# Kernel optimization log

Measured on AMD Instinct MI355X. Metric: run time of the kernel, lower is better.

The kernel has to match this reference:

```python
import jax, jax.numpy as jnp
import numpy as np

NH, NL, NPT = 8, 4, 4  # num_heads, num_levels, num_points


def _bilinear_sample(feat, grid):
    # feat: [N, C, H, W]; grid: [N, S, 2] normalized coords, align_corners=True, zeros padding
    N, C, H, W = feat.shape
    x = (grid[..., 0] + 1.0) * 0.5 * (W - 1)
    y = (grid[..., 1] + 1.0) * 0.5 * (H - 1)
    x0 = jnp.floor(x)
    y0 = jnp.floor(y)
    x1 = x0 + 1.0
    y1 = y0 + 1.0
    wx1 = x - x0
    wx0 = 1.0 - wx1
    wy1 = y - y0
    wy0 = 1.0 - wy1
    flat = feat.reshape(N, C, H * W)

    def corner(xc, yc, wgt):
        valid = (xc >= 0) & (xc <= W - 1) & (yc >= 0) & (yc <= H - 1)
        xi = jnp.clip(xc, 0, W - 1).astype(jnp.int32)
        yi = jnp.clip(yc, 0, H - 1).astype(jnp.int32)
        idx = yi * W + xi  # [N, S]
        vals = jnp.take_along_axis(flat, idx[:, None, :], axis=2)  # [N, C, S]
        return vals * (wgt * valid)[:, None, :]

    return (corner(x0, y0, wx0 * wy0) + corner(x1, y0, wx1 * wy0)
            + corner(x0, y1, wx0 * wy1) + corner(x1, y1, wx1 * wy1))


def _msdeform(query, feats, reference_points, W_off, b_off, W_attn, b_attn, W_out, b_out):
    B, Q, D = query.shape
    hd = D // NH
    offsets = jnp.tanh((query @ W_off + b_off).reshape(B, Q, NH, NL, NPT, 2))
    attn = jax.nn.softmax((query @ W_attn + b_attn).reshape(B, Q, NH, NL * NPT), axis=3)
    attn = attn.reshape(B, Q, NH, NL, NPT)
    ref_grid = reference_points * 2.0 - 1.0  # [B, Q, 2]
    agg = jnp.zeros((B, NH, hd, Q), dtype=query.dtype)
    for lvl, feat in enumerate(feats):
        H, W = feat.shape[2], feat.shape[3]
        f = feat.reshape(B * NH, hd, H, W)
        # [B, NH, Q, P, 2] sampling locations in normalized coords
        grid = ref_grid[:, None, :, None, :] + offsets[:, :, :, lvl].transpose(0, 2, 1, 3, 4)
        grid = grid.reshape(B * NH, Q * NPT, 2)
        sampled = _bilinear_sample(f, grid)  # [B*NH, hd, Q*P]
        sampled = sampled.reshape(B, NH, hd, Q, NPT)
        w = attn[:, :, :, lvl]  # [B, Q, NH, P]
        agg = agg + jnp.einsum('bhcqp,bqhp->bhcq', sampled, w)
    out = agg.transpose(0, 3, 1, 2).reshape(B, Q, D) @ W_out + b_out
    return out, attn


def setup_inputs() -> dict:
    key = jax.random.key(0)
    ks = jax.random.split(key, 12)
    B, Q, D = 2, 21760, 256
    sizes = [(128, 128), (64, 64), (32, 32), (16, 16)]
    inp = {"query": jax.random.normal(ks[0], (B, Q, D), jnp.float32)}
    for i, (H, W) in enumerate(sizes):
        inp[f"feat{i}"] = jax.random.normal(ks[1 + i], (B, D, H, W), jnp.float32)
    inp["reference_points"] = jax.random.uniform(ks[5], (B, Q, 2), dtype=jnp.float32)
    inp["W_off"] = jax.random.normal(ks[6], (D, NH * NL * NPT * 2), jnp.float32) * 0.02
    inp["b_off"] = jax.random.normal(ks[7], (NH * NL * NPT * 2,), jnp.float32) * 0.02
    inp["W_attn"] = jax.random.normal(ks[8], (D, NH * NL * NPT), jnp.float32) * 0.02
    inp["b_attn"] = jax.random.normal(ks[9], (NH * NL * NPT,), jnp.float32) * 0.02
    inp["W_out"] = jax.random.normal(ks[10], (D, D), jnp.float32) * 0.02
    inp["b_out"] = jax.random.normal(ks[11], (D,), jnp.float32) * 0.02
    return inp


def reference(query, feat0, feat1, feat2, feat3, reference_points, W_off, b_off, W_attn, b_attn, W_out, b_out):
    feats = [feat0, feat1, feat2, feat3]
    return _msdeform(query, feats, reference_points, W_off, b_off, W_attn, b_attn, W_out, b_out)
```

## Files before the change

kernel.cpp:

```cpp
#include <hip/hip_runtime.h>
#include <hip/hip_bf16.h>

#define Bn 2
#define Qn 21760
#define BQ 43520
#define HWSUM 21760

typedef __attribute__((ext_vector_type(8))) short bf16x8;
typedef __attribute__((ext_vector_type(4))) float f32x4;

static __device__ __forceinline__ unsigned short f2bf(float f) {
    __hip_bfloat16 h = __float2bfloat16(f);
    return __builtin_bit_cast(unsigned short, h);
}
static __device__ __forceinline__ float bf2f(unsigned short u) {
    return __uint_as_float(((unsigned)u) << 16);
}
static __device__ __forceinline__ void async16(const void* g, void* l) {
    __builtin_amdgcn_global_load_lds(
        (const __attribute__((address_space(1))) unsigned int*)g,
        (__attribute__((address_space(3))) unsigned int*)l, 16, 0, 0);
}

__global__ __launch_bounds__(256) void feat_transpose_kernel(
    const float* __restrict__ f0, const float* __restrict__ f1,
    const float* __restrict__ f2, const float* __restrict__ f3,
    unsigned short* __restrict__ ft)
{
    __shared__ float tile[32][33];
    int bidx = blockIdx.x;
    int b = bidx / 680;
    int pos0 = (bidx - b * 680) * 32;
    int h = blockIdx.y;
    int c0 = h * 32;
    int lvl = (pos0 >= 21504) ? 3 : (pos0 >= 20480) ? 2 : (pos0 >= 16384) ? 1 : 0;
    int HW = 16384 >> (2 * lvl);
    int base = (lvl == 0) ? 0 : (lvl == 1) ? 16384 : (lvl == 2) ? 20480 : 21504;
    const float* f = (lvl == 0) ? f0 : (lvl == 1) ? f1 : (lvl == 2) ? f2 : f3;
    const float* src = f + (size_t)(b * 256 + c0) * HW + (pos0 - base);
    int tx = threadIdx.x & 31, ty = threadIdx.x >> 5;
#pragma unroll
    for (int cc = ty; cc < 32; cc += 8)
        tile[cc][tx] = src[(size_t)cc * HW + tx];
    __syncthreads();
    size_t slab = (size_t)(b * 8 + h) * HWSUM + pos0;
#pragma unroll
    for (int ii = ty; ii < 32; ii += 8)
        ft[(slab + ii) * 32 + tx] = f2bf(tile[tx][ii]);
}

__global__ void zero_hist_kernel(int* hist) { hist[threadIdx.x] = 0; }

static __device__ __forceinline__ int bin_of(const float* refp, int q) {
    float rx = refp[(size_t)q * 2], ry = refp[(size_t)q * 2 + 1];
    int cx = (int)(rx * 16.0f); cx = min(max(cx, 0), 15);
    int cy = (int)(ry * 16.0f); cy = min(max(cy, 0), 15);
    int m = 0;
#pragma unroll
    for (int i = 0; i < 4; ++i)
        m |= (((cx >> i) & 1) << (2 * i)) | (((cy >> i) & 1) << (2 * i + 1));
    return ((q >= Qn) ? 256 : 0) + m;
}

__global__ __launch_bounds__(256) void hist_kernel(
    const float* __restrict__ refp, int* hist)
{
    int q = blockIdx.x * 256 + threadIdx.x;
    if (q < BQ) atomicAdd(&hist[bin_of(refp, q)], 1);
}

__global__ __launch_bounds__(512) void scan_kernel(
    const int* __restrict__ hist, int* cursor)
{
    __shared__ int s[512];
    int t = threadIdx.x;
    int v0 = hist[t];
    s[t] = v0;
    __syncthreads();
    for (int d = 1; d < 512; d <<= 1) {
        int v = (t >= d) ? s[t - d] : 0;
        __syncthreads();
        s[t] += v;
        __syncthreads();
    }
    cursor[t] = s[t] - v0;
}

__global__ __launch_bounds__(256) void scatter_kernel(
    const float* __restrict__ refp, int* cursor, int* order)
{
    int q = blockIdx.x * 256 + threadIdx.x;
    if (q < BQ) {
        int idx = atomicAdd(&cursor[bin_of(refp, q)], 1);
        order[idx] = q;
    }
}

__global__ __launch_bounds__(256) void wsplit_kernel(
    const float* __restrict__ W, unsigned short* __restrict__ bthi,
    unsigned short* __restrict__ btlo, int N, int dolo)
{
    __shared__ float tile[32][33];
    int n0 = blockIdx.x * 32, k0 = blockIdx.y * 32;
    int tx = threadIdx.x & 31, ty = threadIdx.x >> 5;
#pragma unroll
    for (int r = ty; r < 32; r += 8)
        tile[r][tx] = W[(size_t)(k0 + r) * N + n0 + tx];
    __syncthreads();
#pragma unroll
    for (int r = ty; r < 32; r += 8) {
        float v = tile[tx][r];
        unsigned short h = f2bf(v);
        bthi[(size_t)(n0 + r) * 256 + k0 + tx] = h;
        if (dolo) btlo[(size_t)(n0 + r) * 256 + k0 + tx] = f2bf(v - bf2f(h));
    }
}

__global__ __launch_bounds__(256) void qproj_kernel(
    const float* __restrict__ A,
    const unsigned short* __restrict__ wofh, const unsigned short* __restrict__ wofl,
    const unsigned short* __restrict__ watn,
    const float* __restrict__ b_off, const float* __restrict__ b_attn,
    float* __restrict__ offs, float* __restrict__ attn_out)
{
    __shared__ unsigned short Ah[128 * 32], Al[128 * 32];
    __shared__ unsigned short Bh[128 * 32], Bl[128 * 32];
    int tid = threadIdx.x;
    int y = blockIdx.y;
    bool attn = (y == 2);
    int m0 = blockIdx.x * 128;
    const unsigned short* Bhsrc = attn ? watn : (wofh + (size_t)y * 128 * 256);
    const unsigned short* Blsrc = wofl + (size_t)(attn ? 0 : y) * 128 * 256;
    int wave = tid >> 6, lane = tid & 63;
    int wr = wave >> 1, wc = wave & 1;
    int lr = lane & 15, kb = (lane >> 4) * 8;
    int arow = tid >> 2, aseg = (tid & 3) * 8;
    int srow = tid >> 1, sseg = (tid & 1) * 16;
    const float* Ag = A + (size_t)(m0 + srow) * 256 + sseg;
    const unsigned short* Bg  = Bhsrc + (size_t)arow * 256 + aseg;
    const unsigned short* Bg2 = Blsrc + (size_t)arow * 256 + aseg;

    f32x4 acc[4][4] = {};

#define PKPAIR(F0, F1, HP, LP) { \
        unsigned short h0_ = f2bf(F0), h1_ = f2bf(F1); \
        HP = (unsigned)h0_ | ((unsigned)h1_ << 16); \
        LP = (unsigned)f2bf((F0) - bf2f(h0_)) | ((unsigned)f2bf((F1) - bf2f(h1_)) << 16); }

    for (int kt = 0; kt < 256; kt += 32) {
        async16(Bg + kt,            &Bh[tid * 8]);
        async16(Bg + 64 * 256 + kt, &Bh[tid * 8 + 2048]);
        if (!attn) {
            async16(Bg2 + kt,            &Bl[tid * 8]);
            async16(Bg2 + 64 * 256 + kt, &Bl[tid * 8 + 2048]);
        }
        float4 q0 = *(const float4*)(Ag + kt);
        float4 q1 = *(const float4*)(Ag + kt + 4);
        float4 q2 = *(const float4*)(Ag + kt + 8);
        float4 q3 = *(const float4*)(Ag + kt + 12);
        uint4 HP0, HP1, LP0, LP1;
        PKPAIR(q0.x, q0.y, HP0.x, LP0.x); PKPAIR(q0.z, q0.w, HP0.y, LP0.y);
        PKPAIR(q1.x, q1.y, HP0.z, LP0.z); PKPAIR(q1.z, q1.w, HP0.w, LP0.w);
        PKPAIR(q2.x, q2.y, HP1.x, LP1.x); PKPAIR(q2.z, q2.w, HP1.y, LP1.y);
        PKPAIR(q3.x, q3.y, HP1.z, LP1.z); PKPAIR(q3.z, q3.w, HP1.w, LP1.w);
        *(uint4*)&Ah[srow * 32 + sseg]     = HP0;
        *(uint4*)&Ah[srow * 32 + sseg + 8] = HP1;
        if (!attn) {
            *(uint4*)&Al[srow * 32 + sseg]     = LP0;
            *(uint4*)&Al[srow * 32 + sseg + 8] = LP1;
        }
        __syncthreads();
        bf16x8 fah[4], fal[4], fbh[4], fbl[4];
#pragma unroll
        for (int i = 0; i < 4; ++i) {
            fah[i] = *(const bf16x8*)&Ah[(wr * 64 + i * 16 + lr) * 32 + kb];
            fbh[i] = *(const bf16x8*)&Bh[(wc * 64 + i * 16 + lr) * 32 + kb];
        }
        if (!attn) {
#pragma unroll
            for (int i = 0; i < 4; ++i) {
                fal[i] = *(const bf16x8*)&Al[(wr * 64 + i * 16 + lr) * 32 + kb];
                fbl[i] = *(const bf16x8*)&Bl[(wc * 64 + i * 16 + lr) * 32 + kb];
            }
        }
#pragma unroll
        for (int i = 0; i < 4; ++i)
#pragma unroll
            for (int j = 0; j < 4; ++j) {
                acc[i][j] = __builtin_amdgcn_mfma_f32_16x16x32_bf16(
                    fah[i], fbh[j], acc[i][j], 0, 0, 0);
                if (!attn) {
                    acc[i][j] = __builtin_amdgcn_mfma_f32_16x16x32_bf16(
                        fal[i], fbh[j], acc[i][j], 0, 0, 0);
                    acc[i][j] = __builtin_amdgcn_mfma_f32_16x16x32_bf16(
                        fah[i], fbl[j], acc[i][j], 0, 0, 0);
                }
            }
        __syncthreads();
    }

    int crow = (lane >> 4) * 4;
    if (!attn) {
#pragma unroll
        for (int j = 0; j < 4; ++j) {
            int gcol = y * 128 + wc * 64 + j * 16 + lr;
            float bv = b_off[gcol];
#pragma unroll
            for (int i = 0; i < 4; ++i) {
                int grow = m0 + wr * 64 + i * 16 + crow;
#pragma unroll
                for (int r = 0; r < 4; ++r)
                    offs[(size_t)(grow + r) * 256 + gcol] = tanhf(acc[i][j][r] + bv);
            }
        }
    } else {
#pragma unroll
        for (int j = 0; j < 4; ++j) {
            int col = wc * 64 + j * 16 + lr;
            float bv = b_attn[col];
#pragma unroll
            for (int i = 0; i < 4; ++i) {
                int grow = m0 + wr * 64 + i * 16 + crow;
#pragma unroll
                for (int r = 0; r < 4; ++r) {
                    float v = acc[i][j][r] + bv;
                    float mx = v;
                    mx = fmaxf(mx, __shfl_xor(mx, 1));
                    mx = fmaxf(mx, __shfl_xor(mx, 2));
                    mx = fmaxf(mx, __shfl_xor(mx, 4));
                    mx = fmaxf(mx, __shfl_xor(mx, 8));
                    float e = expf(v - mx);
                    float s = e;
                    s += __shfl_xor(s, 1);
                    s += __shfl_xor(s, 2);
                    s += __shfl_xor(s, 4);
                    s += __shfl_xor(s, 8);
                    attn_out[(size_t)(grow + r) * 128 + col] = e / s;
                }
            }
        }
    }
}

__global__ __launch_bounds__(256) void sample_kernel(
    const float* __restrict__ offs, const float* __restrict__ attnw,
    const float* __restrict__ refp, const unsigned short* __restrict__ ft,
    const int* __restrict__ order, unsigned short* __restrict__ aggb)
{
    __shared__ int4   sI[512];
    __shared__ float4 sW[512];
    int tid = threadIdx.x;
    int bid = blockIdx.x;
    int obid = (bid & 7) * 1360 + (bid >> 3);

#pragma unroll
    for (int e = tid; e < 512; e += 256) {
        int qq = e >> 7, pc = e & 127;
        int bq = order[obid * 4 + qq];
        int h = pc >> 4, lvl = (pc >> 2) & 3;
        float2 off = *(const float2*)&offs[((size_t)bq * 128 + pc) * 2];
        float aw = attnw[(size_t)bq * 128 + pc];
        float2 rp = *(const float2*)&refp[(size_t)bq * 2];
        int b = (bq >= Qn) ? 1 : 0;
        int Wl = 128 >> lvl;
        int base = (lvl == 0) ? 0 : (lvl == 1) ? 16384 : (lvl == 2) ? 20480 : 21504;
        float x = (rp.x + 0.5f * off.x) * (float)(Wl - 1);
        float y = (rp.y + 0.5f * off.y) * (float)(Wl - 1);
        float xf = floorf(x), yf = floorf(y);
        int x0 = (int)xf, y0 = (int)yf;
        float wx1 = x - xf, wx0 = 1.0f - wx1;
        float wy1 = y - yf, wy0 = 1.0f - wy1;
        float vx0 = (x0 >= 0 && x0 < Wl) ? 1.0f : 0.0f;
        float vx1 = (x0 + 1 >= 0 && x0 + 1 < Wl) ? 1.0f : 0.0f;
        float vy0 = (y0 >= 0 && y0 < Wl) ? 1.0f : 0.0f;
        float vy1 = (y0 + 1 >= 0 && y0 + 1 < Wl) ? 1.0f : 0.0f;
        int xc0 = min(max(x0, 0), Wl - 1), xc1 = min(max(x0 + 1, 0), Wl - 1);
        int yc0 = min(max(y0, 0), Wl - 1), yc1 = min(max(y0 + 1, 0), Wl - 1);
        int slab = (b * 8 + h) * HWSUM + base;
        int es = e ^ h;
        sI[es] = make_int4((slab + yc0 * Wl + xc0) * 32,
                           (slab + yc1 * Wl + xc0) * 32,
                           (xc1 - xc0) * 32, 0);
        sW[es] = make_float4(wx0 * wy0 * vx0 * vy0 * aw,
                             wx1 * wy0 * vx1 * vy0 * aw,
                             wx0 * wy1 * vx0 * vy1 * aw,
                             wx1 * wy1 * vx1 * vy1 * aw);
    }
    __syncthreads();

    int qq = tid >> 6;
    int h = (tid >> 3) & 7;
    int l = tid & 7;
    int cl = (l & 3) * 8;
    bool hiLane = (l & 4) != 0;
    float a[8] = {};
    int ebase = qq * 128 + h * 16;
#pragma unroll
    for (int j = 0; j < 16; ++j) {
        int es = (ebase + j) ^ h;
        int4 I = sI[es];
        float4 Wv = sW[es];
        int xo = hiLane ? I.z : 0;
        float w0 = hiLane ? Wv.y : Wv.x;
        float w1 = hiLane ? Wv.w : Wv.z;
        uint4 d0 = *(const uint4*)(ft + I.x + xo + cl);
        uint4 d1 = *(const uint4*)(ft + I.y + xo + cl);
        a[0] += w0 * __uint_as_float(d0.x << 16);
        a[1] += w0 * __uint_as_float(d0.x & 0xffff0000u);
        a[2] += w0 * __uint_as_float(d0.y << 16);
        a[3] += w0 * __uint_as_float(d0.y & 0xffff0000u);
        a[4] += w0 * __uint_as_float(d0.z << 16);
        a[5] += w0 * __uint_as_float(d0.z & 0xffff0000u);
        a[6] += w0 * __uint_as_float(d0.w << 16);
        a[7] += w0 * __uint_as_float(d0.w & 0xffff0000u);
        a[0] += w1 * __uint_as_float(d1.x << 16);
        a[1] += w1 * __uint_as_float(d1.x & 0xffff0000u);
        a[2] += w1 * __uint_as_float(d1.y << 16);
        a[3] += w1 * __uint_as_float(d1.y & 0xffff0000u);
        a[4] += w1 * __uint_as_float(d1.z << 16);
        a[5] += w1 * __uint_as_float(d1.z & 0xffff0000u);
        a[6] += w1 * __uint_as_float(d1.w << 16);
        a[7] += w1 * __uint_as_float(d1.w & 0xffff0000u);
    }
#pragma unroll
    for (int k = 0; k < 8; ++k) a[k] += __shfl_xor(a[k], 4);
    if (!hiLane) {
        int bq = order[obid * 4 + qq];
        uint4 o;
        o.x = (unsigned)f2bf(a[0]) | ((unsigned)f2bf(a[1]) << 16);
        o.y = (unsigned)f2bf(a[2]) | ((unsigned)f2bf(a[3]) << 16);
        o.z = (unsigned)f2bf(a[4]) | ((unsigned)f2bf(a[5]) << 16);
        o.w = (unsigned)f2bf(a[6]) | ((unsigned)f2bf(a[7]) << 16);
        *(uint4*)&aggb[(size_t)bq * 256 + h * 32 + cl] = o;
    }
}

__global__ __launch_bounds__(256) void mfma_gemm(
    const unsigned short* __restrict__ Abf, const unsigned short* __restrict__ Bt,
    const float* __restrict__ bias, float* __restrict__ C, int N)
{
    __shared__ unsigned short As[128 * 32];
    __shared__ unsigned short Bs[128 * 32];
    int tid = threadIdx.x;
    int m0 = blockIdx.x * 128, n0 = blockIdx.y * 128;
    int wave = tid >> 6, lane = tid & 63;
    int wr = wave >> 1, wc = wave & 1;
    int lr = lane & 15, kb = (lane >> 4) * 8;
    int arow = tid >> 2, aseg = (tid & 3) * 8;
    const unsigned short* Ag = Abf + (size_t)(m0 + arow) * 256 + aseg;
    const unsigned short* Bg = Bt + (size_t)(n0 + arow) * 256 + aseg;
    f32x4 acc[4][4] = {};
    for (int kt = 0; kt < 256; kt += 32) {
        async16(Ag + kt,            &As[tid * 8]);
        async16(Ag + 64 * 256 + kt, &As[tid * 8 + 2048]);
        async16(Bg + kt,            &Bs[tid * 8]);
        async16(Bg + 64 * 256 + kt, &Bs[tid * 8 + 2048]);
        __syncthreads();
        bf16x8 af[4], bfr[4];
#pragma unroll
        for (int i = 0; i < 4; ++i) {
            af[i]  = *(const bf16x8*)&As[(wr * 64 + i * 16 + lr) * 32 + kb];
            bfr[i] = *(const bf16x8*)&Bs[(wc * 64 + i * 16 + lr) * 32 + kb];
        }
#pragma unroll
        for (int i = 0; i < 4; ++i)
#pragma unroll
            for (int j = 0; j < 4; ++j)
                acc[i][j] = __builtin_amdgcn_mfma_f32_16x16x32_bf16(
                    af[i], bfr[j], acc[i][j], 0, 0, 0);
        __syncthreads();
    }
    int crow = (lane >> 4) * 4;
#pragma unroll
    for (int j = 0; j < 4; ++j) {
        int gcol = n0 + wc * 64 + j * 16 + lr;
        float bv = bias[gcol];
#pragma unroll
        for (int i = 0; i < 4; ++i) {
            int grow = m0 + wr * 64 + i * 16 + crow;
#pragma unroll
            for (int r = 0; r < 4; ++r)
                C[(size_t)(grow + r) * N + gcol] = acc[i][j][r] + bv;
        }
    }
}

extern "C" void kernel_launch(void* const* d_in, const int* in_sizes, int n_in,
                              void* d_out, int out_size, void* d_ws, size_t ws_size,
                              hipStream_t stream)
{
    const float* query  = (const float*)d_in[0];
    const float* f0     = (const float*)d_in[1];
    const float* f1     = (const float*)d_in[2];
    const float* f2     = (const float*)d_in[3];
    const float* f3     = (const float*)d_in[4];
    const float* refp   = (const float*)d_in[5];
    const float* W_off  = (const float*)d_in[6];
    const float* b_off  = (const float*)d_in[7];
    const float* W_attn = (const float*)d_in[8];
    const float* b_attn = (const float*)d_in[9];
    const float* W_out  = (const float*)d_in[10];
    const float* b_out  = (const float*)d_in[11];

    float* out      = (float*)d_out;
    float* attn_out = out + (size_t)BQ * 256;

    char* w = (char*)d_ws;
    float* offs          = (float*)(w + 0);
    unsigned short* ft   = (unsigned short*)(w + 44564480);
    unsigned short* aggb = (unsigned short*)(w + 66846720);
    unsigned short* wofh = (unsigned short*)(w + 89128960);
    unsigned short* wofl = (unsigned short*)(w + 89260032);
    unsigned short* watn = (unsigned short*)(w + 89391104);
    unsigned short* wout = (unsigned short*)(w + 89456640);
    int* hist            = (int*)(w + 89587712);
    int* cursor          = (int*)(w + 89589760);
    int* order           = (int*)(w + 89591808);

    zero_hist_kernel<<<1, 512, 0, stream>>>(hist);
    hist_kernel<<<170, 256, 0, stream>>>(refp, hist);
    scan_kernel<<<1, 512, 0, stream>>>(hist, cursor);
    scatter_kernel<<<170, 256, 0, stream>>>(refp, cursor, order);

    feat_transpose_kernel<<<dim3(1360, 8), 256, 0, stream>>>(f0, f1, f2, f3, ft);
    wsplit_kernel<<<dim3(8, 8), 256, 0, stream>>>(W_off, wofh, wofl, 256, 1);
    wsplit_kernel<<<dim3(4, 8), 256, 0, stream>>>(W_attn, watn, watn, 128, 0);
    wsplit_kernel<<<dim3(8, 8), 256, 0, stream>>>(W_out, wout, wout, 256, 0);

    qproj_kernel<<<dim3(340, 3), 256, 0, stream>>>(
        query, wofh, wofl, watn, b_off, b_attn, offs, attn_out);

    sample_kernel<<<dim3(10880), 256, 0, stream>>>(
        offs, attn_out, refp, ft, order, aggb);

    mfma_gemm<<<dim3(340, 2), 256, 0, stream>>>(aggb, wout, b_out, out, 256);
}
```

Baseline: 204.0 us.

## Fuse offset and attention projections into one wide tile, software-pipeline sampling loads

The query projection now computes all 384 output columns (offsets plus attention logits) in a single 64-row block, so each query tile is loaded and split into hi/lo bf16 once instead of three times, with the concatenated weights staged in LDS. The sampling kernel prefetches gathered feature rows two iterations ahead in a three-slot register ring and accumulates with packed two-wide FMAs, using byte offsets. This aims to cut redundant query reads and hide gather latency, at the cost of higher register and LDS use per block, which may lower occupancy.

```diff
diff --git a/kernel.cpp b/kernel.cpp
--- a/kernel.cpp
+++ b/kernel.cpp
@@ -8,6 +8,7 @@
 
 typedef __attribute__((ext_vector_type(8))) short bf16x8;
 typedef __attribute__((ext_vector_type(4))) float f32x4;
+typedef __attribute__((ext_vector_type(2))) float f32x2;
 
 static __device__ __forceinline__ unsigned short f2bf(float f) {
     __hip_bfloat16 h = __float2bfloat16(f);
@@ -21,6 +22,19 @@
         (const __attribute__((address_space(1))) unsigned int*)g,
         (__attribute__((address_space(3))) unsigned int*)l, 16, 0, 0);
 }
+static __device__ __forceinline__ f32x2 up2(unsigned u) {
+    uint2 t = make_uint2(u << 16, u & 0xffff0000u);
+    return __builtin_bit_cast(f32x2, t);
+}
+static __device__ __forceinline__ f32x2 fma2(float w, f32x2 v, f32x2 a) {
+    f32x2 wv = {w, w};
+    return __builtin_elementwise_fma(wv, v, a);
+}
+
+#define PKPAIR(F0, F1, HP, LP) { \
+        unsigned short h0_ = f2bf(F0), h1_ = f2bf(F1); \
+        HP = (unsigned)h0_ | ((unsigned)h1_ << 16); \
+        LP = (unsigned)f2bf((F0) - bf2f(h0_)) | ((unsigned)f2bf((F1) - bf2f(h1_)) << 16); }
 
 __global__ __launch_bounds__(256) void feat_transpose_kernel(
     const float* __restrict__ f0, const float* __restrict__ f1,
@@ -116,111 +130,95 @@
     }
 }
 
-__global__ __launch_bounds__(256) void qproj_kernel(
+__global__ __launch_bounds__(256, 3) void qproj_kernel(
     const float* __restrict__ A,
-    const unsigned short* __restrict__ wofh, const unsigned short* __restrict__ wofl,
-    const unsigned short* __restrict__ watn,
+    const unsigned short* __restrict__ Wcat,
+    const unsigned short* __restrict__ Wlo,
     const float* __restrict__ b_off, const float* __restrict__ b_attn,
     float* __restrict__ offs, float* __restrict__ attn_out)
 {
-    __shared__ unsigned short Ah[128 * 32], Al[128 * 32];
-    __shared__ unsigned short Bh[128 * 32], Bl[128 * 32];
+    __shared__ unsigned short Ah[64 * 32], Al[64 * 32];
+    __shared__ unsigned short Bh[384 * 32];
+    __shared__ unsigned short Bl[256 * 32];
     int tid = threadIdx.x;
-    int y = blockIdx.y;
-    bool attn = (y == 2);
-    int m0 = blockIdx.x * 128;
-    const unsigned short* Bhsrc = attn ? watn : (wofh + (size_t)y * 128 * 256);
-    const unsigned short* Blsrc = wofl + (size_t)(attn ? 0 : y) * 128 * 256;
+    int m0 = blockIdx.x * 64;
     int wave = tid >> 6, lane = tid & 63;
     int wr = wave >> 1, wc = wave & 1;
     int lr = lane & 15, kb = (lane >> 4) * 8;
-    int arow = tid >> 2, aseg = (tid & 3) * 8;
-    int srow = tid >> 1, sseg = (tid & 1) * 16;
+    int srow = tid >> 2, sseg = (tid & 3) * 8;
     const float* Ag = A + (size_t)(m0 + srow) * 256 + sseg;
-    const unsigned short* Bg  = Bhsrc + (size_t)arow * 256 + aseg;
-    const unsigned short* Bg2 = Blsrc + (size_t)arow * 256 + aseg;
-
-    f32x4 acc[4][4] = {};
-
-#define PKPAIR(F0, F1, HP, LP) { \
-        unsigned short h0_ = f2bf(F0), h1_ = f2bf(F1); \
-        HP = (unsigned)h0_ | ((unsigned)h1_ << 16); \
-        LP = (unsigned)f2bf((F0) - bf2f(h0_)) | ((unsigned)f2bf((F1) - bf2f(h1_)) << 16); }
+
+    f32x4 acc[2][12] = {};
 
     for (int kt = 0; kt < 256; kt += 32) {
-        async16(Bg + kt,            &Bh[tid * 8]);
-        async16(Bg + 64 * 256 + kt, &Bh[tid * 8 + 2048]);
-        if (!attn) {
-            async16(Bg2 + kt,            &Bl[tid * 8]);
-            async16(Bg2 + 64 * 256 + kt, &Bl[tid * 8 + 2048]);
+#pragma unroll
+        for (int p = 0; p < 6; ++p) {
+            int tile = tid + p * 256;
+            int row = tile >> 2, seg = tile & 3;
+            async16(Wcat + (size_t)row * 256 + kt + seg * 8, &Bh[tile * 8]);
+        }
+#pragma unroll
+        for (int p = 0; p < 4; ++p) {
+            int tile = tid + p * 256;
+            int row = tile >> 2, seg = tile & 3;
+            async16(Wlo + (size_t)row * 256 + kt + seg * 8, &Bl[tile * 8]);
         }
         float4 q0 = *(const float4*)(Ag + kt);
         float4 q1 = *(const float4*)(Ag + kt + 4);
-        float4 q2 = *(const float4*)(Ag + kt + 8);
-        float4 q3 = *(const float4*)(Ag + kt + 12);
-        uint4 HP0, HP1, LP0, LP1;
-        PKPAIR(q0.x, q0.y, HP0.x, LP0.x); PKPAIR(q0.z, q0.w, HP0.y, LP0.y);
-        PKPAIR(q1.x, q1.y, HP0.z, LP0.z); PKPAIR(q1.z, q1.w, HP0.w, LP0.w);
-        PKPAIR(q2.x, q2.y, HP1.x, LP1.x); PKPAIR(q2.z, q2.w, HP1.y, LP1.y);
-        PKPAIR(q3.x, q3.y, HP1.z, LP1.z); PKPAIR(q3.z, q3.w, HP1.w, LP1.w);
-        *(uint4*)&Ah[srow * 32 + sseg]     = HP0;
-        *(uint4*)&Ah[srow * 32 + sseg + 8] = HP1;
-        if (!attn) {
-            *(uint4*)&Al[srow * 32 + sseg]     = LP0;
-            *(uint4*)&Al[srow * 32 + sseg + 8] = LP1;
-        }
-        __syncthreads();
-        bf16x8 fah[4], fal[4], fbh[4], fbl[4];
-#pragma unroll
-        for (int i = 0; i < 4; ++i) {
-            fah[i] = *(const bf16x8*)&Ah[(wr * 64 + i * 16 + lr) * 32 + kb];
-            fbh[i] = *(const bf16x8*)&Bh[(wc * 64 + i * 16 + lr) * 32 + kb];
-        }
-        if (!attn) {
-#pragma unroll
-            for (int i = 0; i < 4; ++i) {
-                fal[i] = *(const bf16x8*)&Al[(wr * 64 + i * 16 + lr) * 32 + kb];
-                fbl[i] = *(const bf16x8*)&Bl[(wc * 64 + i * 16 + lr) * 32 + kb];
+        uint4 HP, LP;
+        PKPAIR(q0.x, q0.y, HP.x, LP.x); PKPAIR(q0.z, q0.w, HP.y, LP.y);
+        PKPAIR(q1.x, q1.y, HP.z, LP.z); PKPAIR(q1.z, q1.w, HP.w, LP.w);
+        *(uint4*)&Ah[srow * 32 + sseg] = HP;
+        *(uint4*)&Al[srow * 32 + sseg] = LP;
+        __syncthreads();
+
+        bf16x8 ah[2], al[2];
+#pragma unroll
+        for (int i = 0; i < 2; ++i) {
+            ah[i] = *(const bf16x8*)&Ah[(wr * 32 + i * 16 + lr) * 32 + kb];
+            al[i] = *(const bf16x8*)&Al[(wr * 32 + i * 16 + lr) * 32 + kb];
+        }
+#pragma unroll
+        for (int j = 0; j < 12; ++j) {
+            int c16 = j * 2 + wc;
+            bf16x8 bh = *(const bf16x8*)&Bh[(c16 * 16 + lr) * 32 + kb];
+            if (j < 8) {
+                bf16x8 bl = *(const bf16x8*)&Bl[(c16 * 16 + lr) * 32 + kb];
+#pragma unroll
+                for (int i = 0; i < 2; ++i) {
+                    acc[i][j] = __builtin_amdgcn_mfma_f32_16x16x32_bf16(ah[i], bh, acc[i][j], 0, 0, 0);
+                    acc[i][j] = __builtin_amdgcn_mfma_f32_16x16x32_bf16(al[i], bh, acc[i][j], 0, 0, 0);
+                    acc[i][j] = __builtin_amdgcn_mfma_f32_16x16x32_bf16(ah[i], bl, acc[i][j], 0, 0, 0);
+                }
+            } else {
+#pragma unroll
+                for (int i = 0; i < 2; ++i)
+                    acc[i][j] = __builtin_amdgcn_mfma_f32_16x16x32_bf16(ah[i], bh, acc[i][j], 0, 0, 0);
             }
         }
-#pragma unroll
-        for (int i = 0; i < 4; ++i)
-#pragma unroll
-            for (int j = 0; j < 4; ++j) {
-                acc[i][j] = __builtin_amdgcn_mfma_f32_16x16x32_bf16(
-                    fah[i], fbh[j], acc[i][j], 0, 0, 0);
-                if (!attn) {
-                    acc[i][j] = __builtin_amdgcn_mfma_f32_16x16x32_bf16(
-                        fal[i], fbh[j], acc[i][j], 0, 0, 0);
-                    acc[i][j] = __builtin_amdgcn_mfma_f32_16x16x32_bf16(
-                        fah[i], fbl[j], acc[i][j], 0, 0, 0);
-                }
+        __syncthreads();
+    }
+
+    int crow = (lane >> 4) * 4;
+#pragma unroll
+    for (int j = 0; j < 12; ++j) {
+        int c16 = j * 2 + wc;
+        if (j < 8) {
+            int col = c16 * 16 + lr;
+            float bv = b_off[col];
+#pragma unroll
+            for (int i = 0; i < 2; ++i) {
+                int grow = m0 + wr * 32 + i * 16 + crow;
+#pragma unroll
+                for (int r = 0; r < 4; ++r)
+                    offs[(size_t)(grow + r) * 256 + col] = tanhf(acc[i][j][r] + bv);
             }
-        __syncthreads();
-    }
-
-    int crow = (lane >> 4) * 4;
-    if (!attn) {
-#pragma unroll
-        for (int j = 0; j < 4; ++j) {
-            int gcol = y * 128 + wc * 64 + j * 16 + lr;
-            float bv = b_off[gcol];
-#pragma unroll
-            for (int i = 0; i < 4; ++i) {
-                int grow = m0 + wr * 64 + i * 16 + crow;
-#pragma unroll
-                for (int r = 0; r < 4; ++r)
-                    offs[(size_t)(grow + r) * 256 + gcol] = tanhf(acc[i][j][r] + bv);
-            }
-        }
-    } else {
-#pragma unroll
-        for (int j = 0; j < 4; ++j) {
-            int col = wc * 64 + j * 16 + lr;
+        } else {
+            int col = (c16 - 16) * 16 + lr;
             float bv = b_attn[col];
 #pragma unroll
-            for (int i = 0; i < 4; ++i) {
-                int grow = m0 + wr * 64 + i * 16 + crow;
+            for (int i = 0; i < 2; ++i) {
+                int grow = m0 + wr * 32 + i * 16 + crow;
 #pragma unroll
                 for (int r = 0; r < 4; ++r) {
                     float v = acc[i][j][r] + bv;
@@ -278,9 +276,9 @@
         int yc0 = min(max(y0, 0), Wl - 1), yc1 = min(max(y0 + 1, 0), Wl - 1);
         int slab = (b * 8 + h) * HWSUM + base;
         int es = e ^ h;
-        sI[es] = make_int4((slab + yc0 * Wl + xc0) * 32,
-                           (slab + yc1 * Wl + xc0) * 32,
-                           (xc1 - xc0) * 32, 0);
+        sI[es] = make_int4((slab + yc0 * Wl + xc0) * 64,
+                           (slab + yc1 * Wl + xc0) * 64,
+                           (xc1 - xc0) * 64, 0);
         sW[es] = make_float4(wx0 * wy0 * vx0 * vy0 * aw,
                              wx1 * wy0 * vx1 * vy0 * aw,
                              wx0 * wy1 * vx0 * vy1 * aw,
@@ -291,47 +289,56 @@
     int qq = tid >> 6;
     int h = (tid >> 3) & 7;
     int l = tid & 7;
-    int cl = (l & 3) * 8;
+    int cl2 = (l & 3) * 16;
     bool hiLane = (l & 4) != 0;
-    float a[8] = {};
+    const char* fb = (const char*)ft;
+    f32x2 a01 = {0.f, 0.f}, a23 = {0.f, 0.f}, a45 = {0.f, 0.f}, a67 = {0.f, 0.f};
     int ebase = qq * 128 + h * 16;
+
+    uint4 dX[3], dY[3];
+    float2 wv[3];
+
+#define PREF(J, S) { \
+        int es_ = (ebase + (J)) ^ h; \
+        int4 I_ = sI[es_]; float4 Wf_ = sW[es_]; \
+        int xo_ = (hiLane ? I_.z : 0) + cl2; \
+        wv[S] = hiLane ? make_float2(Wf_.y, Wf_.w) : make_float2(Wf_.x, Wf_.z); \
+        dX[S] = *(const uint4*)(fb + (size_t)(I_.x + xo_)); \
+        dY[S] = *(const uint4*)(fb + (size_t)(I_.y + xo_)); }
+
+    PREF(0, 0);
+    PREF(1, 1);
 #pragma unroll
     for (int j = 0; j < 16; ++j) {
-        int es = (ebase + j) ^ h;
-        int4 I = sI[es];
-        float4 Wv = sW[es];
-        int xo = hiLane ? I.z : 0;
-        float w0 = hiLane ? Wv.y : Wv.x;
-        float w1 = hiLane ? Wv.w : Wv.z;
-        uint4 d0 = *(const uint4*)(ft + I.x + xo + cl);
-        uint4 d1 = *(const uint4*)(ft + I.y + xo + cl);
-        a[0] += w0 * __uint_as_float(d0.x << 16);
-        a[1] += w0 * __uint_as_float(d0.x & 0xffff0000u);
-        a[2] += w0 * __uint_as_float(d0.y << 16);
-        a[3] += w0 * __uint_as_float(d0.y & 0xffff0000u);
-        a[4] += w0 * __uint_as_float(d0.z << 16);
-        a[5] += w0 * __uint_as_float(d0.z & 0xffff0000u);
-        a[6] += w0 * __uint_as_float(d0.w << 16);
-        a[7] += w0 * __uint_as_float(d0.w & 0xffff0000u);
-        a[0] += w1 * __uint_as_float(d1.x << 16);
-        a[1] += w1 * __uint_as_float(d1.x & 0xffff0000u);
-        a[2] += w1 * __uint_as_float(d1.y << 16);
-        a[3] += w1 * __uint_as_float(d1.y & 0xffff0000u);
-        a[4] += w1 * __uint_as_float(d1.z << 16);
-        a[5] += w1 * __uint_as_float(d1.z & 0xffff0000u);
-        a[6] += w1 * __uint_as_float(d1.w << 16);
-        a[7] += w1 * __uint_as_float(d1.w & 0xffff0000u);
-    }
-#pragma unroll
-    for (int k = 0; k < 8; ++k) a[k] += __shfl_xor(a[k], 4);
+        const int s = j % 3;
+        if (j < 14) {
+            const int s2 = (j + 2) % 3;
+            PREF(j + 2, s2);
+        }
+        float w0 = wv[s].x, w1 = wv[s].y;
+        uint4 d0 = dX[s], d1 = dY[s];
+        a01 = fma2(w0, up2(d0.x), a01);
+        a23 = fma2(w0, up2(d0.y), a23);
+        a45 = fma2(w0, up2(d0.z), a45);
+        a67 = fma2(w0, up2(d0.w), a67);
+        a01 = fma2(w1, up2(d1.x), a01);
+        a23 = fma2(w1, up2(d1.y), a23);
+        a45 = fma2(w1, up2(d1.z), a45);
+        a67 = fma2(w1, up2(d1.w), a67);
+    }
+#undef PREF
+
+    float av[8] = {a01.x, a01.y, a23.x, a23.y, a45.x, a45.y, a67.x, a67.y};
+#pragma unroll
+    for (int k = 0; k < 8; ++k) av[k] += __shfl_xor(av[k], 4);
     if (!hiLane) {
         int bq = order[obid * 4 + qq];
         uint4 o;
-        o.x = (unsigned)f2bf(a[0]) | ((unsigned)f2bf(a[1]) << 16);
-        o.y = (unsigned)f2bf(a[2]) | ((unsigned)f2bf(a[3]) << 16);
-        o.z = (unsigned)f2bf(a[4]) | ((unsigned)f2bf(a[5]) << 16);
-        o.w = (unsigned)f2bf(a[6]) | ((unsigned)f2bf(a[7]) << 16);
-        *(uint4*)&aggb[(size_t)bq * 256 + h * 32 + cl] = o;
+        o.x = (unsigned)f2bf(av[0]) | ((unsigned)f2bf(av[1]) << 16);
+        o.y = (unsigned)f2bf(av[2]) | ((unsigned)f2bf(av[3]) << 16);
+        o.z = (unsigned)f2bf(av[4]) | ((unsigned)f2bf(av[5]) << 16);
+        o.w = (unsigned)f2bf(av[6]) | ((unsigned)f2bf(av[7]) << 16);
+        *(uint4*)&aggb[(size_t)bq * 256 + h * 32 + (l & 3) * 8] = o;
     }
 }
 
@@ -409,9 +416,8 @@
     float* offs          = (float*)(w + 0);
     unsigned short* ft   = (unsigned short*)(w + 44564480);
     unsigned short* aggb = (unsigned short*)(w + 66846720);
-    unsigned short* wofh = (unsigned short*)(w + 89128960);
-    unsigned short* wofl = (unsigned short*)(w + 89260032);
-    unsigned short* watn = (unsigned short*)(w + 89391104);
+    unsigned short* Wcat = (unsigned short*)(w + 89128960);
+    unsigned short* Wlo  = (unsigned short*)(w + 89325568);
     unsigned short* wout = (unsigned short*)(w + 89456640);
     int* hist            = (int*)(w + 89587712);
     int* cursor          = (int*)(w + 89589760);
@@ -423,12 +429,12 @@
     scatter_kernel<<<170, 256, 0, stream>>>(refp, cursor, order);
 
     feat_transpose_kernel<<<dim3(1360, 8), 256, 0, stream>>>(f0, f1, f2, f3, ft);
-    wsplit_kernel<<<dim3(8, 8), 256, 0, stream>>>(W_off, wofh, wofl, 256, 1);
-    wsplit_kernel<<<dim3(4, 8), 256, 0, stream>>>(W_attn, watn, watn, 128, 0);
+    wsplit_kernel<<<dim3(8, 8), 256, 0, stream>>>(W_off, Wcat, Wlo, 256, 1);
+    wsplit_kernel<<<dim3(4, 8), 256, 0, stream>>>(W_attn, Wcat + 256 * 256, Wlo, 128, 0);
     wsplit_kernel<<<dim3(8, 8), 256, 0, stream>>>(W_out, wout, wout, 256, 0);
 
-    qproj_kernel<<<dim3(340, 3), 256, 0, stream>>>(
-        query, wofh, wofl, watn, b_off, b_attn, offs, attn_out);
+    qproj_kernel<<<dim3(680), 256, 0, stream>>>(
+        query, Wcat, Wlo, b_off, b_attn, offs, attn_out);
 
     sample_kernel<<<dim3(10880), 256, 0, stream>>>(
         offs, attn_out, refp, ft, order, aggb);
```

Result: faster. 192.8 us (-5.5%).
